# Optimization experiments

Measured on AMD Instinct MI355X. Metric: run time of the kernel, lower is better.

The kernel has to match this reference:

```python
import jax, jax.numpy as jnp
import numpy as np

B, N, K = 32, 64, 128          # batch, atoms per cell, channel width (128x0e + 128x1o)
R_MAX = 5.0
NUM_BESSEL = 8
P_CUT = 5                       # num_polynomial_cutoff
AVG_NEIGH = 16.0                # avg_num_neighbors
H_MLP = 512                     # hidden_dimensions_size, n_hidden_dimensions = 2
FEAT = 5 * K                    # ((num_interactions-1)*4 + 1) * 128 = 640


def silu(x):
    return x * jax.nn.sigmoid(x)


def _bessel_cutoff(r, mask):
    # Bessel radial basis * polynomial cutoff (MACE), masked on valid edges.
    n = jnp.arange(1, NUM_BESSEL + 1, dtype=r.dtype)
    rb = jnp.sqrt(2.0 / R_MAX) * jnp.sin(n * (jnp.pi / R_MAX) * r[..., None]) / r[..., None]
    u = r / R_MAX
    p = float(P_CUT)
    fc = 1.0 - 0.5 * (p + 1) * (p + 2) * u**P_CUT + p * (p + 2) * u**(P_CUT + 1) - 0.5 * p * (p + 1) * u**(P_CUT + 2)
    fc = fc * (u < 1.0)
    return rb * (fc * mask)[..., None]


def _sph(uvec):
    # Real spherical harmonics l=0,1,2 (component normalization), uvec: unit edge vectors.
    x, y, z = uvec[..., 0], uvec[..., 1], uvec[..., 2]
    s3, s5, s15 = 3.0**0.5, 5.0**0.5, 15.0**0.5
    Y0 = jnp.ones_like(x)[..., None]
    Y1 = jnp.stack([s3 * x, s3 * y, s3 * z], -1)
    Y2 = jnp.stack([s15 * x * y, s15 * y * z, 0.5 * s5 * (3 * z * z - 1.0),
                    s15 * x * z, 0.5 * s15 * (x * x - y * y)], -1)
    return Y0, Y1, Y2


def _radial_mlp(x, w0, b0, w1, b1, w2, b2, w3, b3):
    h = silu(x @ w0 + b0)
    h = silu(h @ w1 + b1)
    h = silu(h @ w2 + b2)
    return h @ w3 + b3


def setup_inputs() -> dict:
    key = jax.random.key(0)
    ks = jax.random.split(key, 32)
    f32 = jnp.float32

    def lin(k, fan_in, shape):
        return (jax.random.normal(k, shape, dtype=f32) / np.sqrt(fan_in)).astype(f32)

    inp = {
        "noisy_relative_positions": jax.random.uniform(ks[0], (B, N, 3), dtype=f32),
        "time": jax.random.uniform(ks[1], (B, 1), dtype=f32),
        "unit_cell": (11.0 * jnp.eye(3, dtype=f32) + 0.3 * jax.random.uniform(ks[2], (B, 3, 3), dtype=f32)),
        "w_embed": lin(ks[3], 1, (K,)),
        # interaction 1 radial MLP: 8 -> 64 -> 64 -> 64 -> 3*K (weights for l=0,1,2 paths)
        "r1_w0": lin(ks[4], NUM_BESSEL, (NUM_BESSEL, 64)), "r1_b0": jnp.zeros((64,), f32),
        "r1_w1": lin(ks[5], 64, (64, 64)), "r1_b1": jnp.zeros((64,), f32),
        "r1_w2": lin(ks[6], 64, (64, 64)), "r1_b2": jnp.zeros((64,), f32),
        "r1_w3": lin(ks[7], 64, (64, 3 * K)), "r1_b3": jnp.zeros((3 * K,), f32),
        "mix1_l0": lin(ks[8], K, (K, K)),
        "mix1_l1": lin(ks[9], K, (K, K)),
        "mix1_l2": lin(ks[10], K, (K, K)),
        # interaction 2 radial MLP: 8 -> 64 -> 64 -> 64 -> 2*K (paths 0e x 0e -> 0e, 1o x 1o -> 0e)
        "r2_w0": lin(ks[11], NUM_BESSEL, (NUM_BESSEL, 64)), "r2_b0": jnp.zeros((64,), f32),
        "r2_w1": lin(ks[12], 64, (64, 64)), "r2_b1": jnp.zeros((64,), f32),
        "r2_w2": lin(ks[13], 64, (64, 64)), "r2_b2": jnp.zeros((64,), f32),
        "r2_w3": lin(ks[14], 64, (64, 2 * K)), "r2_b3": jnp.zeros((2 * K,), f32),
        "mix2": lin(ks[15], K, (K, K)),
        # readout MLP: 641 -> 512 -> 512 -> 3
        "mlp_w0": lin(ks[16], FEAT + 1, (FEAT + 1, H_MLP)), "mlp_b0": jnp.zeros((H_MLP,), f32),
        "mlp_w1": lin(ks[17], H_MLP, (H_MLP, H_MLP)), "mlp_b1": jnp.zeros((H_MLP,), f32),
        "mlp_w2": lin(ks[18], H_MLP, (H_MLP, 3)), "mlp_b2": jnp.zeros((3,), f32),
    }
    return inp


def reference(noisy_relative_positions, time, unit_cell, w_embed,
              r1_w0, r1_b0, r1_w1, r1_b1, r1_w2, r1_b2, r1_w3, r1_b3,
              mix1_l0, mix1_l1, mix1_l2,
              r2_w0, r2_b0, r2_w1, r2_b1, r2_w2, r2_b2, r2_w3, r2_b3, mix2,
              mlp_w0, mlp_b0, mlp_w1, mlp_b1, mlp_w2, mlp_b2):
    frac = noisy_relative_positions                      # [B,N,3] fractional
    d = frac[:, :, None, :] - frac[:, None, :, :]        # [B,N,N,3]
    d = d - jnp.round(d)                                 # minimum-image PBC
    dc = jnp.einsum('bijc,bcd->bijd', d, unit_cell)      # cartesian displacements
    r = jnp.sqrt(jnp.maximum(jnp.sum(dc * dc, -1), 1e-12))
    mask = (r < R_MAX) & (~jnp.eye(N, dtype=bool))[None]
    r_safe = jnp.where(mask, r, 1.0)
    uvec = dc / r_safe[..., None] * mask[..., None]      # unit edge vectors (0 off-edge)

    rad = _bessel_cutoff(r_safe, mask)                   # [B,N,N,8]
    Y0, Y1, Y2 = _sph(uvec)                              # [B,N,N,1|3|5]

    h0 = jnp.broadcast_to(w_embed, (B, N, K))            # element embedding (single species)

    # ---- interaction 1: radial-weighted tensor product h_j (x) Y_l, scatter over j ----
    we = _radial_mlp(rad, r1_w0, r1_b0, r1_w1, r1_b1, r1_w2, r1_b2, r1_w3, r1_b3)
    we = we.reshape(B, N, N, 3, K) * mask[..., None, None]
    hj = h0[:, None, :, :]                               # sender features [B,1,N,K]
    msg0 = jnp.einsum('bijk,bijm->bimk', we[..., 0, :] * hj, Y0)[:, :, 0] / AVG_NEIGH  # [B,N,K]
    msg1 = jnp.einsum('bijk,bijm->bimk', we[..., 1, :] * hj, Y1) / AVG_NEIGH           # [B,N,3,K]
    msg2 = jnp.einsum('bijk,bijm->bimk', we[..., 2, :] * hj, Y2) / AVG_NEIGH           # [B,N,5,K]

    s1 = msg0 @ mix1_l0 + jnp.sum(msg2 * msg2, axis=2) @ mix1_l2   # scalars [B,N,K]
    v1 = jnp.einsum('bimk,kc->bimc', msg1, mix1_l1)                # vectors [B,N,3,K]
    h1 = silu(s1)

    # ---- interaction 2: scalar output from 0e x 0e and 1o x 1o -> 0e paths ----
    we2 = _radial_mlp(rad, r2_w0, r2_b0, r2_w1, r2_b1, r2_w2, r2_b2, r2_w3, r2_b3)
    we2 = we2.reshape(B, N, N, 2, K) * mask[..., None, None]
    msg_a = jnp.sum(we2[..., 0, :] * h1[:, None, :, :], axis=2)    # [B,N,K]
    inv = jnp.einsum('bijm,bjmk->bijk', Y1, v1)                    # Y1 . v1_j invariant
    msg_b = jnp.sum(we2[..., 1, :] * inv, axis=2)
    s2 = ((msg_a + msg_b) / AVG_NEIGH) @ mix2                      # [B,N,K]

    # node_feats: layer1 full irreps (128x0e + 128x1o -> 512) + layer2 scalars (128) = 640
    node_feats = jnp.concatenate([s1, v1.reshape(B, N, 3 * K), s2], axis=-1)

    t = jnp.broadcast_to(time[:, None, :], (B, N, 1))
    x = jnp.concatenate([node_feats, t], axis=-1)                  # [B,N,641]
    x = jax.nn.relu(x @ mlp_w0 + mlp_b0)
    x = jax.nn.relu(x @ mlp_w1 + mlp_b1)
    return x @ mlp_w2 + mlp_b2                                     # [B,N,3]
```

## Files before the change

kernel.cpp:

```cpp
#include <hip/hip_runtime.h>
#include <math.h>

#define B_ 32
#define N_ 64
#define K_ 128
#define NPAIR (B_*N_*N_)

typedef __attribute__((ext_vector_type(8))) short short8;
typedef __attribute__((ext_vector_type(8))) __bf16 bf16x8;
typedef __attribute__((ext_vector_type(4))) float floatx4;

__device__ __forceinline__ float silu_f(float x) {
    return x / (1.0f + expf(-x));
}
__device__ __forceinline__ float4 ld4(const float* p) { return *(const float4*)p; }

__device__ __forceinline__ short f2bf(float x) {
    union { float f; unsigned u; } v; v.f = x;
    unsigned r = (v.u + 0x7FFFu + ((v.u >> 16) & 1u)) >> 16;
    return (short)r;
}
__device__ __forceinline__ float bf2f(short s) {
    union { unsigned u; float f; } v;
    v.u = ((unsigned)(unsigned short)s) << 16;
    return v.f;
}
__device__ __forceinline__ bf16x8 ld_frag(const short* p) {
    short8 r = *(const short8*)p;
    return __builtin_bit_cast(bf16x8, r);
}

__global__ __launch_bounds__(256) void prep_kernel(
    const float* __restrict__ r1w1, const float* __restrict__ r1w2,
    const float* __restrict__ r2w1, const float* __restrict__ r2w2,
    const float* __restrict__ r2w3, const float* __restrict__ mw0,
    const float* __restrict__ mw1, short* __restrict__ dst)
{
    int idx = blockIdx.x * 256 + threadIdx.x;
    if (idx >= 655360) return;
    short v;
    if (idx < 4096) {
        int h = idx >> 6, k = idx & 63; v = f2bf(r1w1[k*64 + h]);
    } else if (idx < 8192) {
        int i = idx - 4096; int h = i >> 6, k = i & 63; v = f2bf(r1w2[k*64 + h]);
    } else if (idx < 12288) {
        int i = idx - 8192; int h = i >> 6, k = i & 63; v = f2bf(r2w1[k*64 + h]);
    } else if (idx < 16384) {
        int i = idx - 12288; int h = i >> 6, k = i & 63; v = f2bf(r2w2[k*64 + h]);
    } else if (idx < 32768) {
        int i = idx - 16384; int col = i >> 6, h = i & 63; v = f2bf(r2w3[h*256 + col]);
    } else if (idx < 393216) {
        int i = idx - 32768; int n = i / 704, k = i - n*704;
        v = (k < 641) ? f2bf(mw0[(size_t)k*512 + n]) : (short)0;
    } else {
        int i = idx - 393216; int n = i >> 9, k = i & 511;
        v = f2bf(mw1[(size_t)k*512 + n]);
    }
    dst[idx] = v;
}

__global__ __launch_bounds__(256) void geom_kernel(
    const float* __restrict__ pos, const float* __restrict__ cell,
    float* __restrict__ rad, float* __restrict__ Y1, float* __restrict__ Y2,
    float* __restrict__ maskf)
{
    int p = blockIdx.x * 256 + threadIdx.x;
    if (p >= NPAIR) return;
    int b = p >> 12;
    int ij = p & 4095;
    int i = ij >> 6, j = ij & 63;
    const float* pi = pos + (size_t)(b*N_ + i)*3;
    const float* pj = pos + (size_t)(b*N_ + j)*3;
    float d0 = pi[0]-pj[0], d1 = pi[1]-pj[1], d2 = pi[2]-pj[2];
    d0 -= rintf(d0); d1 -= rintf(d1); d2 -= rintf(d2);
    const float* C = cell + b*9;
    float dc0 = d0*C[0] + d1*C[3] + d2*C[6];
    float dc1 = d0*C[1] + d1*C[4] + d2*C[7];
    float dc2 = d0*C[2] + d1*C[5] + d2*C[8];
    float r2 = fmaxf(dc0*dc0 + dc1*dc1 + dc2*dc2, 1e-12f);
    float r = sqrtf(r2);
    bool m = (r < 5.0f) && (i != j);
    float mf = m ? 1.0f : 0.0f;
    float rs = m ? r : 1.0f;
    float inv_rs = 1.0f / rs;
    float x = dc0*inv_rs*mf, y = dc1*inv_rs*mf, z = dc2*inv_rs*mf;
    float u = r * 0.2f;
    float u2 = u*u, u4 = u2*u2, u5 = u4*u;
    float fc = 1.0f - 21.0f*u5 + 35.0f*u5*u - 15.0f*u5*u2;
    fc = (u < 1.0f) ? fc : 0.0f;
    float pref = 0.6324555320336759f * inv_rs * (fc * mf);
    float w = 0.6283185307179586f * rs;
    #pragma unroll
    for (int n = 1; n <= 8; n++)
        rad[(size_t)p*8 + (n-1)] = pref * sinf((float)n * w);
    const float s3  = 1.7320508075688772f;
    const float s5  = 2.23606797749979f;
    const float s15 = 3.872983346207417f;
    float* y1 = Y1 + (size_t)p*3;
    y1[0] = s3*x; y1[1] = s3*y; y1[2] = s3*z;
    float* y2 = Y2 + (size_t)p*5;
    y2[0] = s15*x*y;
    y2[1] = s15*y*z;
    y2[2] = 0.5f*s5*(3.0f*z*z - 1.0f);
    y2[3] = s15*x*z;
    y2[4] = 0.5f*s15*(x*x - y*y);
    maskf[p] = mf;
}

__device__ __forceinline__ void mfma_layer(
    const short* __restrict__ src, const short* __restrict__ WT,
    const float* __restrict__ bias, short* __restrict__ dst,
    int wv, int qd, int nn)
{
    floatx4 acc[4];
    #pragma unroll
    for (int tt = 0; tt < 4; tt++) acc[tt] = (floatx4){0.f, 0.f, 0.f, 0.f};
    #pragma unroll
    for (int ks = 0; ks < 64; ks += 32) {
        bf16x8 a = ld_frag(&src[(wv*16 + nn)*72 + ks + qd*8]);
        #pragma unroll
        for (int tt = 0; tt < 4; tt++) {
            bf16x8 b = ld_frag(&WT[(tt*16 + nn)*64 + ks + qd*8]);
            acc[tt] = __builtin_amdgcn_mfma_f32_16x16x32_bf16(a, b, acc[tt], 0, 0, 0);
        }
    }
    #pragma unroll
    for (int tt = 0; tt < 4; tt++) {
        int col = tt*16 + nn;
        float bv = bias[col];
        #pragma unroll
        for (int i = 0; i < 4; i++) {
            int row = wv*16 + qd*4 + i;
            dst[row*72 + col] = f2bf(silu_f(acc[tt][i] + bv));
        }
    }
}

__global__ __launch_bounds__(256) void pass1_kernel(
    const float* __restrict__ rad, const float* __restrict__ Y1g,
    const float* __restrict__ Y2g, const float* __restrict__ maskg,
    const float* __restrict__ wemb,
    const float* __restrict__ w0, const float* __restrict__ b0,
    const short* __restrict__ w1T, const float* __restrict__ b1,
    const short* __restrict__ w2T, const float* __restrict__ b2,
    const float* __restrict__ w3, const float* __restrict__ b3,
    const float* __restrict__ l0, const float* __restrict__ l1,
    const float* __restrict__ l2, const float* __restrict__ timeg,
    float* __restrict__ h1g, float* __restrict__ v1g, short* __restrict__ featsb)
{
    __shared__ float rad_s[512];
    __shared__ short actA[64*72];
    __shared__ short actB[64*72];
    __shared__ float Ym[9*64];
    __shared__ float G[9*64];
    __shared__ float SY[9];
    __shared__ float msg[9*128];
    __shared__ float q_s[128];
    int t = threadIdx.x;
    int wv = t >> 6, lane = t & 63, qd = lane >> 4, nn = lane & 15;
    int node = blockIdx.x;
    int b = node >> 6;
    size_t pbase = (size_t)node * 64;

    for (int idx = t; idx < 512; idx += 256) rad_s[idx] = rad[pbase*8 + idx];
    if (t < 64) {
        int j = t;
        float mf = maskg[pbase + j];
        Ym[j] = mf;
        #pragma unroll
        for (int m = 0; m < 3; m++) Ym[(1+m)*64 + j] = Y1g[(pbase+j)*3 + m] * mf;
        #pragma unroll
        for (int m = 0; m < 5; m++) Ym[(4+m)*64 + j] = Y2g[(pbase+j)*5 + m] * mf;
    }
    __syncthreads();

    for (int idx = t; idx < 4096; idx += 256) {
        int j = idx >> 6, h = idx & 63;
        float acc = b0[h];
        #pragma unroll
        for (int c = 0; c < 8; c++) acc += rad_s[j*8+c] * w0[c*64+h];
        actA[j*72 + h] = f2bf(silu_f(acc));
    }
    __syncthreads();
    mfma_layer(actA, w1T, b1, actB, wv, qd, nn);
    __syncthreads();
    mfma_layer(actB, w2T, b2, actA, wv, qd, nn);
    __syncthreads();

    if (t < 9) {
        float acc = 0.f;
        for (int j = 0; j < 64; j++) acc += Ym[t*64 + j];
        SY[t] = acc;
    }
    for (int idx = t; idx < 576; idx += 256) {
        int m = idx >> 6, h = idx & 63;
        float acc = 0.f;
        #pragma unroll 8
        for (int j = 0; j < 64; j++) acc += Ym[m*64 + j] * bf2f(actA[j*72 + h]);
        G[m*64 + h] = acc;
    }
    __syncthreads();

    for (int idx = t; idx < 1152; idx += 256) {
        int m = idx >> 7, k = idx & 127;
        int c = (m == 0) ? 0 : ((m < 4) ? 1 : 2);
        int col = c*128 + k;
        float acc = SY[m] * b3[col];
        #pragma unroll 8
        for (int h = 0; h < 64; h++) acc += G[m*64 + h] * w3[h*384 + col];
        msg[m*128 + k] = acc * wemb[k] * 0.0625f;
    }
    __syncthreads();

    if (t < 128) {
        int k = t;
        float acc = 0.f;
        #pragma unroll
        for (int m = 4; m < 9; m++) { float v = msg[m*128 + k]; acc += v*v; }
        q_s[k] = acc;
    }
    __syncthreads();

    for (int idx = t; idx < 512; idx += 256) {
        if (idx < 128) {
            int c = idx;
            float acc = 0.f;
            for (int k = 0; k < 128; k++)
                acc += msg[k]*l0[k*128 + c] + q_s[k]*l2[k*128 + c];
            featsb[(size_t)node*704 + c] = f2bf(acc);
            h1g[(size_t)node*128 + c] = silu_f(acc);
        } else {
            int vi = idx - 128;
            int m = vi >> 7, c = vi & 127;
            float acc = 0.f;
            for (int k = 0; k < 128; k++) acc += msg[(1+m)*128 + k]*l1[k*128 + c];
            v1g[(size_t)node*384 + m*128 + c] = acc;
            featsb[(size_t)node*704 + 128 + m*128 + c] = f2bf(acc);
        }
    }
    if (t == 0) featsb[(size_t)node*704 + 640] = f2bf(timeg[b]);
    if (t < 63) featsb[(size_t)node*704 + 641 + t] = 0;
}

__global__ __launch_bounds__(256) void pass2_kernel(
    const float* __restrict__ rad, const float* __restrict__ Y1g,
    const float* __restrict__ maskg,
    const float* __restrict__ w0, const float* __restrict__ b0,
    const short* __restrict__ w1T, const float* __restrict__ b1,
    const short* __restrict__ w2T, const float* __restrict__ b2,
    const short* __restrict__ w3T, const float* __restrict__ b3,
    const float* __restrict__ mix2,
    const float* __restrict__ h1g, const float* __restrict__ v1g,
    short* __restrict__ featsb)
{
    __shared__ float rad_s[512];
    __shared__ short actA[64*72];
    __shared__ short actB[64*72];
    __shared__ float Y1s[64*4];
    __shared__ float mask_s[64];
    __shared__ float msgab[128];
    int t = threadIdx.x;
    int wv = t >> 6, lane = t & 63, qd = lane >> 4, nn = lane & 15;
    int node = blockIdx.x;
    int b = node >> 6;
    size_t pbase = (size_t)node * 64;

    for (int idx = t; idx < 512; idx += 256) rad_s[idx] = rad[pbase*8 + idx];
    if (t < 64) {
        mask_s[t] = maskg[pbase + t];
        #pragma unroll
        for (int m = 0; m < 3; m++) Y1s[t*4 + m] = Y1g[(pbase+t)*3 + m];
    }
    if (t < 128) msgab[t] = 0.f;
    __syncthreads();

    for (int idx = t; idx < 4096; idx += 256) {
        int j = idx >> 6, h = idx & 63;
        float acc = b0[h];
        #pragma unroll
        for (int c = 0; c < 8; c++) acc += rad_s[j*8+c] * w0[c*64+h];
        actA[j*72 + h] = f2bf(silu_f(acc));
    }
    __syncthreads();
    mfma_layer(actA, w1T, b1, actB, wv, qd, nn);
    __syncthreads();
    mfma_layer(actB, w2T, b2, actA, wv, qd, nn);
    __syncthreads();

    for (int g = 0; g < 4; g++) {
        floatx4 acc[4];
        #pragma unroll
        for (int tt = 0; tt < 4; tt++) acc[tt] = (floatx4){0.f, 0.f, 0.f, 0.f};
        #pragma unroll
        for (int ks = 0; ks < 64; ks += 32) {
            bf16x8 a = ld_frag(&actA[(wv*16 + nn)*72 + ks + qd*8]);
            #pragma unroll
            for (int tt = 0; tt < 4; tt++) {
                int col0 = g*64 + tt*16;
                bf16x8 bb = ld_frag(&w3T[(col0 + nn)*64 + ks + qd*8]);
                acc[tt] = __builtin_amdgcn_mfma_f32_16x16x32_bf16(a, bb, acc[tt], 0, 0, 0);
            }
        }
        #pragma unroll
        for (int tt = 0; tt < 4; tt++) {
            int col = g*64 + tt*16 + nn;
            float bias = b3[col];
            int k = col & 127;
            float p = 0.f;
            if (col < 128) {
                #pragma unroll
                for (int i = 0; i < 4; i++) {
                    int j = wv*16 + qd*4 + i;
                    float we = (acc[tt][i] + bias) * mask_s[j];
                    p += we * h1g[((size_t)b*64 + j)*128 + k];
                }
            } else {
                #pragma unroll
                for (int i = 0; i < 4; i++) {
                    int j = wv*16 + qd*4 + i;
                    float we = (acc[tt][i] + bias) * mask_s[j];
                    const float* vb = &v1g[((size_t)b*64 + j)*384 + k];
                    float inv = Y1s[j*4+0]*vb[0] + Y1s[j*4+1]*vb[128] + Y1s[j*4+2]*vb[256];
                    p += we * inv;
                }
            }
            p += __shfl_xor(p, 16);
            p += __shfl_xor(p, 32);
            if (qd == 0) atomicAdd(&msgab[k], p);
        }
    }
    __syncthreads();

    if (t < 128) {
        int c = t;
        float acc = 0.f;
        for (int k = 0; k < 128; k++) acc += msgab[k] * mix2[k*128 + c];
        featsb[(size_t)node*704 + 512 + c] = f2bf(acc * 0.0625f);
    }
}

__global__ __launch_bounds__(256) void gemm_mfma_kernel(
    const short* __restrict__ A, int lda,
    const short* __restrict__ BT, int ldb, int K,
    const float* __restrict__ bias, short* __restrict__ Cout, int ldo)
{
    __shared__ short As[64*72];
    __shared__ short Bs[64*72];
    int t = threadIdx.x;
    int wv = t >> 6, lane = t & 63, qd = lane >> 4, nn = lane & 15;
    int m0 = blockIdx.x * 64, n0 = blockIdx.y * 64;
    floatx4 acc[4];
    #pragma unroll
    for (int tt = 0; tt < 4; tt++) acc[tt] = (floatx4){0.f, 0.f, 0.f, 0.f};

    for (int kc = 0; kc < K; kc += 64) {
        for (int s = t; s < 512; s += 256) {
            int j = s >> 3, kk = (s & 7) * 8;
            *(uint4*)&As[j*72 + kk] = *(const uint4*)&A[(size_t)(m0 + j)*lda + kc + kk];
            *(uint4*)&Bs[j*72 + kk] = *(const uint4*)&BT[(size_t)(n0 + j)*ldb + kc + kk];
        }
        __syncthreads();
        #pragma unroll
        for (int ks = 0; ks < 64; ks += 32) {
            bf16x8 a = ld_frag(&As[(wv*16 + nn)*72 + ks + qd*8]);
            #pragma unroll
            for (int tt = 0; tt < 4; tt++) {
                bf16x8 bb = ld_frag(&Bs[(tt*16 + nn)*72 + ks + qd*8]);
                acc[tt] = __builtin_amdgcn_mfma_f32_16x16x32_bf16(a, bb, acc[tt], 0, 0, 0);
            }
        }
        __syncthreads();
    }
    #pragma unroll
    for (int tt = 0; tt < 4; tt++) {
        int n = n0 + tt*16 + nn;
        float bv = bias[n];
        #pragma unroll
        for (int i = 0; i < 4; i++) {
            int m = m0 + wv*16 + qd*4 + i;
            Cout[(size_t)m*ldo + n] = f2bf(fmaxf(acc[tt][i] + bv, 0.f));
        }
    }
}

__global__ __launch_bounds__(64) void final3_kernel(
    const short* __restrict__ H, const float* __restrict__ w2,
    const float* __restrict__ b2, float* __restrict__ out)
{
    int node = blockIdx.x, lane = threadIdx.x;
    float a0 = 0.f, a1 = 0.f, a2 = 0.f;
    #pragma unroll
    for (int r = 0; r < 8; r++) {
        int k = r*64 + lane;
        float h = bf2f(H[(size_t)node*512 + k]);
        a0 += h * w2[k*3 + 0];
        a1 += h * w2[k*3 + 1];
        a2 += h * w2[k*3 + 2];
    }
    #pragma unroll
    for (int off = 32; off > 0; off >>= 1) {
        a0 += __shfl_down(a0, off);
        a1 += __shfl_down(a1, off);
        a2 += __shfl_down(a2, off);
    }
    if (lane == 0) {
        out[(size_t)node*3 + 0] = a0 + b2[0];
        out[(size_t)node*3 + 1] = a1 + b2[1];
        out[(size_t)node*3 + 2] = a2 + b2[2];
    }
}

extern "C" void kernel_launch(void* const* d_in, const int* in_sizes, int n_in,
                              void* d_out, int out_size, void* d_ws, size_t ws_size,
                              hipStream_t stream) {
    const float* pos   = (const float*)d_in[0];
    const float* timeg = (const float*)d_in[1];
    const float* cell  = (const float*)d_in[2];
    const float* wemb  = (const float*)d_in[3];
    const float* r1w0  = (const float*)d_in[4];
    const float* r1b0  = (const float*)d_in[5];
    const float* r1w1  = (const float*)d_in[6];
    const float* r1b1  = (const float*)d_in[7];
    const float* r1w2  = (const float*)d_in[8];
    const float* r1b2  = (const float*)d_in[9];
    const float* r1w3  = (const float*)d_in[10];
    const float* r1b3  = (const float*)d_in[11];
    const float* l0    = (const float*)d_in[12];
    const float* l1    = (const float*)d_in[13];
    const float* l2    = (const float*)d_in[14];
    const float* r2w0  = (const float*)d_in[15];
    const float* r2b0  = (const float*)d_in[16];
    const float* r2w1  = (const float*)d_in[17];
    const float* r2b1  = (const float*)d_in[18];
    const float* r2w2  = (const float*)d_in[19];
    const float* r2b2  = (const float*)d_in[20];
    const float* r2w3  = (const float*)d_in[21];
    const float* r2b3  = (const float*)d_in[22];
    const float* mix2  = (const float*)d_in[23];
    const float* mw0   = (const float*)d_in[24];
    const float* mb0   = (const float*)d_in[25];
    const float* mw1   = (const float*)d_in[26];
    const float* mb1   = (const float*)d_in[27];
    const float* mw2   = (const float*)d_in[28];
    const float* mb2   = (const float*)d_in[29];

    float* ws    = (float*)d_ws;
    float* rad   = ws;
    float* Y1    = rad   + (size_t)NPAIR*8;
    float* Y2    = Y1    + (size_t)NPAIR*3;
    float* maskf = Y2    + (size_t)NPAIR*5;
    float* h1    = maskf + (size_t)NPAIR;
    float* v1    = h1    + (size_t)B_*N_*K_;
    short* featsb = (short*)(v1 + (size_t)B_*N_*3*K_);
    short* prep  = featsb + (size_t)2048*704;
    short* w1T_1 = prep;
    short* w2T_1 = prep + 4096;
    short* w1T_2 = prep + 8192;
    short* w2T_2 = prep + 12288;
    short* w3T_2 = prep + 16384;
    short* wT0   = prep + 32768;
    short* wT1   = prep + 393216;
    short* h0bb = (short*)rad;
    short* h1bb = (short*)Y2;

    prep_kernel<<<(655360 + 255)/256, 256, 0, stream>>>(
        r1w1, r1w2, r2w1, r2w2, r2w3, mw0, mw1, prep);
    geom_kernel<<<NPAIR/256, 256, 0, stream>>>(pos, cell, rad, Y1, Y2, maskf);
    pass1_kernel<<<B_*N_, 256, 0, stream>>>(rad, Y1, Y2, maskf, wemb,
        r1w0, r1b0, w1T_1, r1b1, w2T_1, r1b2, r1w3, r1b3, l0, l1, l2, timeg,
        h1, v1, featsb);
    pass2_kernel<<<B_*N_, 256, 0, stream>>>(rad, Y1, maskf,
        r2w0, r2b0, w1T_2, r2b1, w2T_2, r2b2, w3T_2, r2b3, mix2, h1, v1, featsb);
    dim3 g0(32, 8);
    gemm_mfma_kernel<<<g0, 256, 0, stream>>>(featsb, 704, wT0, 704, 704, mb0, h0bb, 512);
    gemm_mfma_kernel<<<g0, 256, 0, stream>>>(h0bb, 512, wT1, 512, 512, mb1, h1bb, 512);
    final3_kernel<<<B_*N_, 64, 0, stream>>>(h1bb, mw2, mb2, (float*)d_out);
}
```

Baseline: 285.5 us.

## Move pass1 radial first layer, projections and mixing onto bf16 MFMA

Replaces the scalar fp32 loops in pass1 with bf16 MFMA tiles for the first radial layer (padded to K=32), the Y-weighted neighbour reduction G, the w3 projection, and the l0/l1/l2 channel mixing, which is packed as one concatenated transposed weight. Pass2's first layer also moves to MFMA. The prep kernel pre-transposes and converts these extra weights to bf16, and the SY sums now use wave shuffles. This removes long per-thread serial FMA loops over shared and global memory. In exchange, more intermediates (G, messages, radial inputs) are rounded to bf16, which costs accuracy.

```diff
diff --git a/kernel.cpp b/kernel.cpp
--- a/kernel.cpp
+++ b/kernel.cpp
@@ -5,6 +5,7 @@
 #define N_ 64
 #define K_ 128
 #define NPAIR (B_*N_*N_)
+#define PREP_TOTAL 733184
 
 typedef __attribute__((ext_vector_type(8))) short short8;
 typedef __attribute__((ext_vector_type(8))) __bf16 bf16x8;
@@ -13,7 +14,6 @@
 __device__ __forceinline__ float silu_f(float x) {
     return x / (1.0f + expf(-x));
 }
-__device__ __forceinline__ float4 ld4(const float* p) { return *(const float4*)p; }
 
 __device__ __forceinline__ short f2bf(float x) {
     union { float f; unsigned u; } v; v.f = x;
@@ -34,10 +34,15 @@
     const float* __restrict__ r1w1, const float* __restrict__ r1w2,
     const float* __restrict__ r2w1, const float* __restrict__ r2w2,
     const float* __restrict__ r2w3, const float* __restrict__ mw0,
-    const float* __restrict__ mw1, short* __restrict__ dst)
+    const float* __restrict__ mw1,
+    const float* __restrict__ r1w0, const float* __restrict__ r2w0,
+    const float* __restrict__ r1w3,
+    const float* __restrict__ l0, const float* __restrict__ l1,
+    const float* __restrict__ l2,
+    short* __restrict__ dst)
 {
     int idx = blockIdx.x * 256 + threadIdx.x;
-    if (idx >= 655360) return;
+    if (idx >= PREP_TOTAL) return;
     short v;
     if (idx < 4096) {
         int h = idx >> 6, k = idx & 63; v = f2bf(r1w1[k*64 + h]);
@@ -52,9 +57,24 @@
     } else if (idx < 393216) {
         int i = idx - 32768; int n = i / 704, k = i - n*704;
         v = (k < 641) ? f2bf(mw0[(size_t)k*512 + n]) : (short)0;
-    } else {
+    } else if (idx < 655360) {
         int i = idx - 393216; int n = i >> 9, k = i & 511;
         v = f2bf(mw1[(size_t)k*512 + n]);
+    } else if (idx < 657408) {
+        int i = idx - 655360; int h = i >> 5, k = i & 31;
+        v = (k < 8) ? f2bf(r1w0[k*64 + h]) : (short)0;
+    } else if (idx < 659456) {
+        int i = idx - 657408; int h = i >> 5, k = i & 31;
+        v = (k < 8) ? f2bf(r2w0[k*64 + h]) : (short)0;
+    } else if (idx < 684032) {
+        int i = idx - 659456; int col = i >> 6, h = i & 63;
+        v = f2bf(r1w3[(size_t)h*384 + col]);
+    } else {
+        int i = idx - 684032; int n = i >> 7, k = i & 127;
+        float src = (n < 128) ? l0[(size_t)k*128 + n]
+                  : (n < 256) ? l1[(size_t)k*128 + (n-128)]
+                              : l2[(size_t)k*128 + (n-256)];
+        v = f2bf(src);
     }
     dst[idx] = v;
 }
@@ -136,25 +156,79 @@
     }
 }
 
+__device__ __forceinline__ void mfma_layer_T(
+    const short* __restrict__ src, const short* __restrict__ WT,
+    const float* __restrict__ bias, short* __restrict__ dstT,
+    int wv, int qd, int nn)
+{
+    floatx4 acc[4];
+    #pragma unroll
+    for (int tt = 0; tt < 4; tt++) acc[tt] = (floatx4){0.f, 0.f, 0.f, 0.f};
+    #pragma unroll
+    for (int ks = 0; ks < 64; ks += 32) {
+        bf16x8 a = ld_frag(&src[(wv*16 + nn)*72 + ks + qd*8]);
+        #pragma unroll
+        for (int tt = 0; tt < 4; tt++) {
+            bf16x8 b = ld_frag(&WT[(tt*16 + nn)*64 + ks + qd*8]);
+            acc[tt] = __builtin_amdgcn_mfma_f32_16x16x32_bf16(a, b, acc[tt], 0, 0, 0);
+        }
+    }
+    #pragma unroll
+    for (int tt = 0; tt < 4; tt++) {
+        int col = tt*16 + nn;
+        float bv = bias[col];
+        #pragma unroll
+        for (int i = 0; i < 4; i++) {
+            int row = wv*16 + qd*4 + i;
+            dstT[col*72 + row] = f2bf(silu_f(acc[tt][i] + bv));
+        }
+    }
+}
+
+__device__ __forceinline__ void mfma_layer0(
+    const short* __restrict__ rad_bf, const short* __restrict__ w0T,
+    const float* __restrict__ b0, short* __restrict__ dst,
+    int wv, int qd, int nn)
+{
+    floatx4 acc[4];
+    #pragma unroll
+    for (int tt = 0; tt < 4; tt++) acc[tt] = (floatx4){0.f, 0.f, 0.f, 0.f};
+    bf16x8 a = ld_frag(&rad_bf[(wv*16 + nn)*40 + qd*8]);
+    #pragma unroll
+    for (int tt = 0; tt < 4; tt++) {
+        bf16x8 b = ld_frag(&w0T[(tt*16 + nn)*32 + qd*8]);
+        acc[tt] = __builtin_amdgcn_mfma_f32_16x16x32_bf16(a, b, acc[tt], 0, 0, 0);
+    }
+    #pragma unroll
+    for (int tt = 0; tt < 4; tt++) {
+        int col = tt*16 + nn;
+        float bv = b0[col];
+        #pragma unroll
+        for (int i = 0; i < 4; i++) {
+            int row = wv*16 + qd*4 + i;
+            dst[row*72 + col] = f2bf(silu_f(acc[tt][i] + bv));
+        }
+    }
+}
+
 __global__ __launch_bounds__(256) void pass1_kernel(
     const float* __restrict__ rad, const float* __restrict__ Y1g,
     const float* __restrict__ Y2g, const float* __restrict__ maskg,
     const float* __restrict__ wemb,
-    const float* __restrict__ w0, const float* __restrict__ b0,
+    const short* __restrict__ w0T, const float* __restrict__ b0,
     const short* __restrict__ w1T, const float* __restrict__ b1,
     const short* __restrict__ w2T, const float* __restrict__ b2,
-    const float* __restrict__ w3, const float* __restrict__ b3,
-    const float* __restrict__ l0, const float* __restrict__ l1,
-    const float* __restrict__ l2, const float* __restrict__ timeg,
+    const short* __restrict__ w3T, const float* __restrict__ b3,
+    const short* __restrict__ lcatT, const float* __restrict__ timeg,
     float* __restrict__ h1g, float* __restrict__ v1g, short* __restrict__ featsb)
 {
-    __shared__ float rad_s[512];
-    __shared__ short actA[64*72];
-    __shared__ short actB[64*72];
-    __shared__ float Ym[9*64];
-    __shared__ float G[9*64];
+    __shared__ __align__(16) short lds_a[2560];
+    __shared__ __align__(16) short actA[64*72];
+    __shared__ __align__(16) short actB[64*72];
+    __shared__ __align__(16) short Ym_bf[16*72];
+    __shared__ __align__(16) short G_bf[16*72];
+    __shared__ __align__(16) float msg[1152];
     __shared__ float SY[9];
-    __shared__ float msg[9*128];
     __shared__ float q_s[128];
     int t = threadIdx.x;
     int wv = t >> 6, lane = t & 63, qd = lane >> 4, nn = lane & 15;
@@ -162,53 +236,81 @@
     int b = node >> 6;
     size_t pbase = (size_t)node * 64;
 
-    for (int idx = t; idx < 512; idx += 256) rad_s[idx] = rad[pbase*8 + idx];
+    for (int idx = t; idx < 2048; idx += 256) {
+        int j = idx >> 5, k = idx & 31;
+        lds_a[j*40 + k] = (k < 8) ? f2bf(rad[pbase*8 + j*8 + k]) : (short)0;
+    }
     if (t < 64) {
         int j = t;
         float mf = maskg[pbase + j];
-        Ym[j] = mf;
-        #pragma unroll
-        for (int m = 0; m < 3; m++) Ym[(1+m)*64 + j] = Y1g[(pbase+j)*3 + m] * mf;
-        #pragma unroll
-        for (int m = 0; m < 5; m++) Ym[(4+m)*64 + j] = Y2g[(pbase+j)*5 + m] * mf;
-    }
-    __syncthreads();
-
-    for (int idx = t; idx < 4096; idx += 256) {
-        int j = idx >> 6, h = idx & 63;
-        float acc = b0[h];
-        #pragma unroll
-        for (int c = 0; c < 8; c++) acc += rad_s[j*8+c] * w0[c*64+h];
-        actA[j*72 + h] = f2bf(silu_f(acc));
-    }
+        float vals[9];
+        vals[0] = mf;
+        #pragma unroll
+        for (int m = 0; m < 3; m++) vals[1+m] = Y1g[(pbase+j)*3 + m] * mf;
+        #pragma unroll
+        for (int m = 0; m < 5; m++) vals[4+m] = Y2g[(pbase+j)*5 + m] * mf;
+        #pragma unroll
+        for (int m = 0; m < 9; m++) Ym_bf[m*72 + j] = f2bf(vals[m]);
+        #pragma unroll
+        for (int m = 9; m < 16; m++) Ym_bf[m*72 + j] = 0;
+        #pragma unroll
+        for (int m = 0; m < 9; m++) {
+            float s = vals[m];
+            #pragma unroll
+            for (int off = 32; off > 0; off >>= 1) s += __shfl_xor(s, off);
+            if (j == 0) SY[m] = s;
+        }
+    }
+    __syncthreads();
+
+    mfma_layer0(lds_a, w0T, b0, actA, wv, qd, nn);
     __syncthreads();
     mfma_layer(actA, w1T, b1, actB, wv, qd, nn);
     __syncthreads();
-    mfma_layer(actB, w2T, b2, actA, wv, qd, nn);
-    __syncthreads();
-
-    if (t < 9) {
-        float acc = 0.f;
-        for (int j = 0; j < 64; j++) acc += Ym[t*64 + j];
-        SY[t] = acc;
-    }
-    for (int idx = t; idx < 576; idx += 256) {
-        int m = idx >> 6, h = idx & 63;
-        float acc = 0.f;
-        #pragma unroll 8
-        for (int j = 0; j < 64; j++) acc += Ym[m*64 + j] * bf2f(actA[j*72 + h]);
-        G[m*64 + h] = acc;
-    }
-    __syncthreads();
-
-    for (int idx = t; idx < 1152; idx += 256) {
-        int m = idx >> 7, k = idx & 127;
-        int c = (m == 0) ? 0 : ((m < 4) ? 1 : 2);
-        int col = c*128 + k;
-        float acc = SY[m] * b3[col];
-        #pragma unroll 8
-        for (int h = 0; h < 64; h++) acc += G[m*64 + h] * w3[h*384 + col];
-        msg[m*128 + k] = acc * wemb[k] * 0.0625f;
+    mfma_layer_T(actB, w2T, b2, actA, wv, qd, nn);
+    __syncthreads();
+
+    {
+        floatx4 acc = (floatx4){0.f, 0.f, 0.f, 0.f};
+        #pragma unroll
+        for (int ks = 0; ks < 64; ks += 32) {
+            bf16x8 a = ld_frag(&Ym_bf[nn*72 + ks + qd*8]);
+            bf16x8 bb = ld_frag(&actA[(wv*16 + nn)*72 + ks + qd*8]);
+            acc = __builtin_amdgcn_mfma_f32_16x16x32_bf16(a, bb, acc, 0, 0, 0);
+        }
+        #pragma unroll
+        for (int i = 0; i < 4; i++)
+            G_bf[(qd*4 + i)*72 + wv*16 + nn] = f2bf(acc[i]);
+    }
+    __syncthreads();
+
+    {
+        floatx4 acc[6];
+        #pragma unroll
+        for (int tt = 0; tt < 6; tt++) acc[tt] = (floatx4){0.f, 0.f, 0.f, 0.f};
+        #pragma unroll
+        for (int ks = 0; ks < 64; ks += 32) {
+            bf16x8 a = ld_frag(&G_bf[nn*72 + ks + qd*8]);
+            #pragma unroll
+            for (int tt = 0; tt < 6; tt++) {
+                bf16x8 bb = ld_frag(&w3T[((wv*6 + tt)*16 + nn)*64 + ks + qd*8]);
+                acc[tt] = __builtin_amdgcn_mfma_f32_16x16x32_bf16(a, bb, acc[tt], 0, 0, 0);
+            }
+        }
+        #pragma unroll
+        for (int tt = 0; tt < 6; tt++) {
+            int col = (wv*6 + tt)*16 + nn;
+            #pragma unroll
+            for (int i = 0; i < 4; i++) {
+                int m = qd*4 + i;
+                if (m < 9) {
+                    int c = (m == 0) ? 0 : ((m < 4) ? 1 : 2);
+                    int k = col - c*128;
+                    if (k >= 0 && k < 128)
+                        msg[m*128 + k] = (acc[tt][i] + SY[m]*b3[col]) * wemb[k] * 0.0625f;
+                }
+            }
+        }
     }
     __syncthreads();
 
@@ -221,21 +323,59 @@
     }
     __syncthreads();
 
+    for (int idx = t; idx < 2048; idx += 256) {
+        int r = idx >> 7, k = idx & 127;
+        float v = (r == 0) ? msg[k]
+                : (r == 1) ? q_s[k]
+                : (r < 5)  ? msg[(r-1)*128 + k] : 0.f;
+        lds_a[r*136 + k] = f2bf(v);
+    }
+    __syncthreads();
+
+    {
+        floatx4 acc[6];
+        #pragma unroll
+        for (int tt = 0; tt < 6; tt++) acc[tt] = (floatx4){0.f, 0.f, 0.f, 0.f};
+        #pragma unroll
+        for (int ks = 0; ks < 128; ks += 32) {
+            bf16x8 a = ld_frag(&lds_a[nn*136 + ks + qd*8]);
+            #pragma unroll
+            for (int tt = 0; tt < 6; tt++) {
+                bf16x8 bb = ld_frag(&lcatT[((size_t)((wv*6 + tt)*16 + nn))*128 + ks + qd*8]);
+                acc[tt] = __builtin_amdgcn_mfma_f32_16x16x32_bf16(a, bb, acc[tt], 0, 0, 0);
+            }
+        }
+        float* Ps_a = msg;
+        float* Ps_b = msg + 128;
+        float* Pv   = msg + 256;
+        #pragma unroll
+        for (int tt = 0; tt < 6; tt++) {
+            int n = (wv*6 + tt)*16 + nn;
+            #pragma unroll
+            for (int i = 0; i < 4; i++) {
+                int r = qd*4 + i;
+                float val = acc[tt][i];
+                if (r == 0 && n < 128) Ps_a[n] = val;
+                else if (r == 1 && n >= 256) Ps_b[n - 256] = val;
+                else if (r >= 2 && r < 5 && n >= 128 && n < 256)
+                    Pv[(r-2)*128 + (n-128)] = val;
+            }
+        }
+    }
+    __syncthreads();
+
     for (int idx = t; idx < 512; idx += 256) {
         if (idx < 128) {
             int c = idx;
-            float acc = 0.f;
-            for (int k = 0; k < 128; k++)
-                acc += msg[k]*l0[k*128 + c] + q_s[k]*l2[k*128 + c];
-            featsb[(size_t)node*704 + c] = f2bf(acc);
-            h1g[(size_t)node*128 + c] = silu_f(acc);
+            float s1 = msg[c] + msg[128 + c];
+            featsb[(size_t)node*704 + c] = f2bf(s1);
+            h1g[(size_t)node*128 + c] = silu_f(s1);
         } else {
             int vi = idx - 128;
             int m = vi >> 7, c = vi & 127;
-            float acc = 0.f;
-            for (int k = 0; k < 128; k++) acc += msg[(1+m)*128 + k]*l1[k*128 + c];
-            v1g[(size_t)node*384 + m*128 + c] = acc;
-            featsb[(size_t)node*704 + 128 + m*128 + c] = f2bf(acc);
+            float v = msg[256 + m*128 + c];
+            v1g[(size_t)node*384 + m*128 + c] = v;
+            featsb[(size_t)node*704 + 128 + m*128 + c] = f2bf(v);
         }
     }
     if (t == 0) featsb[(size_t)node*704 + 640] = f2bf(timeg[b]);
@@ -245,7 +385,7 @@
 __global__ __launch_bounds__(256) void pass2_kernel(
     const float* __restrict__ rad, const float* __restrict__ Y1g,
     const float* __restrict__ maskg,
-    const float* __restrict__ w0, const float* __restrict__ b0,
+    const short* __restrict__ w0T, const float* __restrict__ b0,
     const short* __restrict__ w1T, const float* __restrict__ b1,
     const short* __restrict__ w2T, const float* __restrict__ b2,
     const short* __restrict__ w3T, const float* __restrict__ b3,
@@ -253,9 +393,9 @@
     const float* __restrict__ h1g, const float* __restrict__ v1g,
     short* __restrict__ featsb)
 {
-    __shared__ float rad_s[512];
-    __shared__ short actA[64*72];
-    __shared__ short actB[64*72];
+    __shared__ __align__(16) short rad_bf[2560];
+    __shared__ __align__(16) short actA[64*72];
+    __shared__ __align__(16) short actB[64*72];
     __shared__ float Y1s[64*4];
     __shared__ float mask_s[64];
     __shared__ float msgab[128];
@@ -265,7 +405,10 @@
     int b = node >> 6;
     size_t pbase = (size_t)node * 64;
 
-    for (int idx = t; idx < 512; idx += 256) rad_s[idx] = rad[pbase*8 + idx];
+    for (int idx = t; idx < 2048; idx += 256) {
+        int j = idx >> 5, k = idx & 31;
+        rad_bf[j*40 + k] = (k < 8) ? f2bf(rad[pbase*8 + j*8 + k]) : (short)0;
+    }
     if (t < 64) {
         mask_s[t] = maskg[pbase + t];
         #pragma unroll
@@ -274,13 +417,7 @@
     if (t < 128) msgab[t] = 0.f;
     __syncthreads();
 
-    for (int idx = t; idx < 4096; idx += 256) {
-        int j = idx >> 6, h = idx & 63;
-        float acc = b0[h];
-        #pragma unroll
-        for (int c = 0; c < 8; c++) acc += rad_s[j*8+c] * w0[c*64+h];
-        actA[j*72 + h] = f2bf(silu_f(acc));
-    }
+    mfma_layer0(rad_bf, w0T, b0, actA, wv, qd, nn);
     __syncthreads();
     mfma_layer(actA, w1T, b1, actB, wv, qd, nn);
     __syncthreads();
@@ -460,17 +597,22 @@
     short* w3T_2 = prep + 16384;
     short* wT0   = prep + 32768;
     short* wT1   = prep + 393216;
+    short* w0T_1 = prep + 655360;
+    short* w0T_2 = prep + 657408;
+    short* w3T_1 = prep + 659456;
+    short* lcatT = prep + 684032;
     short* h0bb = (short*)rad;
     short* h1bb = (short*)Y2;
 
-    prep_kernel<<<(655360 + 255)/256, 256, 0, stream>>>(
-        r1w1, r1w2, r2w1, r2w2, r2w3, mw0, mw1, prep);
+    prep_kernel<<<(PREP_TOTAL + 255)/256, 256, 0, stream>>>(
+        r1w1, r1w2, r2w1, r2w2, r2w3, mw0, mw1,
+        r1w0, r2w0, r1w3, l0, l1, l2, prep);
     geom_kernel<<<NPAIR/256, 256, 0, stream>>>(pos, cell, rad, Y1, Y2, maskf);
     pass1_kernel<<<B_*N_, 256, 0, stream>>>(rad, Y1, Y2, maskf, wemb,
-        r1w0, r1b0, w1T_1, r1b1, w2T_1, r1b2, r1w3, r1b3, l0, l1, l2, timeg,
+        w0T_1, r1b0, w1T_1, r1b1, w2T_1, r1b2, w3T_1, r1b3, lcatT, timeg,
         h1, v1, featsb);
     pass2_kernel<<<B_*N_, 256, 0, stream>>>(rad, Y1, maskf,
-        r2w0, r2b0, w1T_2, r2b1, w2T_2, r2b2, w3T_2, r2b3, mix2, h1, v1, featsb);
+        w0T_2, r2b0, w1T_2, r2b1, w2T_2, r2b2, w3T_2, r2b3, mix2, h1, v1, featsb);
     dim3 g0(32, 8);
     gemm_mfma_kernel<<<g0, 256, 0, stream>>>(featsb, 704, wT0, 704, 704, mb0, h0bb, 512);
     gemm_mfma_kernel<<<g0, 256, 0, stream>>>(h0bb, 512, wT1, 512, 512, mb1, h1bb, 512);
```

Measured after the change: 289.2 us. Within noise of the previous version (+1.3%).
